# Performance work log

Hardware: AMD Instinct MI355X
Metric: run time of the kernel (lower is better)

The kernel has to match this reference:

```python
import jax, jax.numpy as jnp
import numpy as np

N = 262144
C = 4096  # number of clusters


def _segment_max(x, seg, num_segments):
    # global_max_pool: per-cluster max over points
    return jax.ops.segment_max(x, seg, num_segments=num_segments)


def setup_inputs() -> dict:
    key = jax.random.key(0)
    ks = jax.random.split(key, 16)

    def lin(k, fan_in, fan_out):
        bound = 1.0 / np.sqrt(fan_in)
        kw, kb = jax.random.split(k)
        W = jax.random.uniform(kw, (fan_in, fan_out), jnp.float32, -bound, bound)
        b = jax.random.uniform(kb, (fan_out,), jnp.float32, -bound, bound)
        return W, b

    relative_points = jax.random.normal(ks[0], (N, 3), jnp.float32)
    features = jax.random.normal(ks[1], (N, 64), jnp.float32)
    cluster = jax.random.randint(ks[2], (N,), 0, C, jnp.int64)

    enc_W1, enc_b1 = lin(ks[3], 3, 32)    # neighborhood encoder MLP
    enc_W2, enc_b2 = lin(ks[4], 32, 64)
    W1, b1 = lin(ks[5], 3 + 64 + 64, 128)  # fc_layers (input_size + enc_out + 3)
    W2, b2 = lin(ks[6], 128, 128)
    G1, gb1 = lin(ks[7], 128, 128)          # fc_layers_global
    G2, gb2 = lin(ks[8], 128, 256)

    return dict(relative_points=relative_points, features=features, cluster=cluster,
                enc_W1=enc_W1, enc_b1=enc_b1, enc_W2=enc_W2, enc_b2=enc_b2,
                W1=W1, b1=b1, W2=W2, b2=b2, G1=G1, gb1=gb1, G2=G2, gb2=gb2)


def reference(relative_points, features, cluster,
              enc_W1, enc_b1, enc_W2, enc_b2,
              W1, b1, W2, b2, G1, gb1, G2, gb2):
    # --- neighborhood encoder: per-point MLP then per-cluster max-pool ---
    h = jax.nn.relu(relative_points @ enc_W1 + enc_b1)          # [N, 32]
    h = jax.nn.relu(h @ enc_W2 + enc_b2)                        # [N, 64]
    neigh_enc = _segment_max(h, cluster, C)                     # [C, 64]

    # gather-by-index duplication + concat
    dup = neigh_enc[cluster]                                    # [N, 64]
    encoded = jnp.concatenate([relative_points, features, dup], axis=1)  # [N, 131]

    # local fc stack (relu, leaky=False)
    encoded = jax.nn.relu(encoded @ W1 + b1)                    # [N, 128]
    encoded = jax.nn.relu(encoded @ W2 + b2)                    # [N, 128]

    # global_max_pool (mean=False)
    encoded_global = _segment_max(encoded, cluster, C)          # [C, 128]

    # global fc stack
    encoded_global = jax.nn.relu(encoded_global @ G1 + gb1)     # [C, 128]
    encoded_global = jax.nn.relu(encoded_global @ G2 + gb2)     # [C, 256]
    return encoded_global
```

## Files before the change

### kernel.cpp

```cpp
#include <hip/hip_runtime.h>

#define NN 262144
#define CC 4096
#define NBLK 64
#define PPB (NN / NBLK)
#define NT (NN / 64)
#define SLOTS 3

typedef __attribute__((ext_vector_type(8))) short bf16x8;
typedef __attribute__((ext_vector_type(4))) float f32x4;

__device__ __forceinline__ unsigned short f_to_bf16u(float f) {
  union { float f; unsigned u; } v; v.f = f;
  unsigned u = v.u;
  u += 0x7fffu + ((u >> 16) & 1u);
  return (unsigned short)(u >> 16);
}
__device__ __forceinline__ unsigned pk2(float a, float b) {
  return (unsigned)f_to_bf16u(a) | ((unsigned)f_to_bf16u(b) << 16);
}

__global__ __launch_bounds__(256) void k_hist(
    const int* __restrict__ cluster, unsigned* __restrict__ hist2d)
{
  __shared__ unsigned h[CC];
  const int t = threadIdx.x, b = blockIdx.x;
  for (int q = t; q < CC; q += 256) h[q] = 0u;
  __syncthreads();
  const int base = b * PPB;
#pragma unroll 4
  for (int k = 0; k < PPB; k += 256) atomicAdd(&h[cluster[base + k + t]], 1u);
  __syncthreads();
  for (int q = t; q < CC; q += 256) hist2d[b * CC + q] = h[q];
}

__global__ __launch_bounds__(256) void k_scan_a(
    const unsigned* __restrict__ hist2d, unsigned* __restrict__ base2d,
    unsigned* __restrict__ totals)
{
  const int c = blockIdx.x * 256 + threadIdx.x;
  unsigned acc = 0;
#pragma unroll 4
  for (int b = 0; b < NBLK; ++b) {
    const unsigned v = hist2d[b * CC + c];
    base2d[b * CC + c] = acc;
    acc += v;
  }
  totals[c] = acc;
}

__global__ __launch_bounds__(256) void k_scan_b(
    const unsigned* __restrict__ totals, unsigned* __restrict__ cstart)
{
  __shared__ unsigned part[256];
  const int t = threadIdx.x;
  unsigned loc[16];
  unsigned s = 0;
#pragma unroll
  for (int q = 0; q < 16; ++q) { loc[q] = s; s += totals[t * 16 + q]; }
  part[t] = s;
  __syncthreads();
  for (int off = 1; off < 256; off <<= 1) {
    const unsigned v = (t >= off) ? part[t - off] : 0u;
    __syncthreads();
    part[t] += v;
    __syncthreads();
  }
  const unsigned baset = part[t] - s;
#pragma unroll
  for (int q = 0; q < 16; ++q) cstart[t * 16 + q] = baset + loc[q];
}

__global__ __launch_bounds__(256) void k_scatter(
    const int* __restrict__ cluster, const unsigned* __restrict__ base2d,
    const unsigned* __restrict__ cstart, unsigned* __restrict__ perm,
    unsigned* __restrict__ scid)
{
  __shared__ unsigned cur[CC];
  const int t = threadIdx.x, b = blockIdx.x;
  for (int q = t; q < CC; q += 256) cur[q] = base2d[b * CC + q] + cstart[q];
  __syncthreads();
  const int base = b * PPB;
#pragma unroll 4
  for (int k = 0; k < PPB; k += 256) {
    const int i = base + k + t;
    const int c = cluster[i];
    const unsigned pos = atomicAdd(&cur[c], 1u);
    perm[pos] = (unsigned)i;
    scid[pos] = (unsigned)c;
  }
}

__global__ __launch_bounds__(256) void k_pack(
    const float* __restrict__ eW2, const float* __restrict__ W1,
    const float* __restrict__ W2, unsigned* __restrict__ packE,
    unsigned* __restrict__ pack1, unsigned* __restrict__ pack2)
{
  const int id = blockIdx.x * 256 + threadIdx.x;
  if (id < 1024) {
    const int nt = id >> 8, l = (id >> 2) & 63, v = id & 3;
    const int k0 = (l >> 4) * 8 + 2 * v, col = nt * 16 + (l & 15);
    packE[id] = pk2(eW2[k0 * 64 + col], eW2[(k0 + 1) * 64 + col]);
  } else if (id < 1024 + 6144) {
    const int j = id - 1024;
    const int kk = j >> 11, nt = (j >> 8) & 7, l = (j >> 2) & 63, v = j & 3;
    const int col = nt * 16 + (l & 15);
    float vals[2];
#pragma unroll
    for (int h = 0; h < 2; ++h) {
      const int k = kk * 32 + (l >> 4) * 8 + 2 * v + h;
      vals[h] = (k < 64) ? W1[(3 + k) * 128 + col]
              : (k < 67) ? W1[(k - 64) * 128 + col] : 0.f;
    }
    pack1[j] = pk2(vals[0], vals[1]);
  } else if (id < 1024 + 6144 + 8192) {
    const int j = id - (1024 + 6144);
    const int kk = j >> 11, nt = (j >> 8) & 7, l = (j >> 2) & 63, v = j & 3;
    const int col = nt * 16 + (l & 15);
    const int k0 = kk * 32 + (l >> 4) * 4 + v;
    pack2[j] = pk2(W2[k0 * 128 + col], W2[(k0 + 16) * 128 + col]);
  }
}

__global__ __launch_bounds__(256) void k_enc_t(
    const float* __restrict__ pts, const unsigned* __restrict__ perm,
    const unsigned* __restrict__ scid, const unsigned* __restrict__ cstart,
    const float* __restrict__ eW1, const float* __restrict__ eb1,
    const float* __restrict__ eb2, const unsigned* __restrict__ packE,
    float* __restrict__ pse)
{
  __shared__ float P4[64 * 4];
  __shared__ unsigned h1s[64 * 20];
  __shared__ int seg_r0[65];
  __shared__ int seg_cid[64];
  __shared__ int seg_j[64];
  __shared__ int nseg_s;
  const int t = threadIdx.x;
  const int lane = t & 63, w = t >> 6;
  const int g = lane >> 4, ln15 = lane & 15;
  const int b = blockIdx.x;

  if (w == 0) {
    const int cid = (int)scid[b * 64 + t];
    const bool flag = (t == 0) || ((int)scid[b * 64 + t - 1] != cid);
    const unsigned long long mask = __ballot(flag);
    const int rank = (int)__popcll(mask & ((1ull << t) - 1ull));
    if (flag) {
      seg_r0[rank] = t;
      seg_cid[rank] = cid;
      seg_j[rank] = b - (int)(cstart[cid] >> 6);
    }
    if (t == 0) {
      const int ns = (int)__popcll(mask);
      nseg_s = ns;
      seg_r0[ns] = 64;
    }
    const int i = (int)perm[b * 64 + t];
    P4[t * 4 + 0] = pts[i * 3 + 0];
    P4[t * 4 + 1] = pts[i * 3 + 1];
    P4[t * 4 + 2] = pts[i * 3 + 2];
    P4[t * 4 + 3] = 0.f;
  }
  __syncthreads();
  {
    const int r = t >> 2, qq = t & 3;
    const float p0 = P4[r * 4], p1 = P4[r * 4 + 1], p2 = P4[r * 4 + 2];
    unsigned wv[4];
#pragma unroll
    for (int u = 0; u < 4; ++u) {
      float hv[2];
#pragma unroll
      for (int hh = 0; hh < 2; ++hh) {
        const int cc2 = qq * 8 + 2 * u + hh;
        hv[hh] = fmaxf(fmaf(p2, eW1[64 + cc2],
                       fmaf(p1, eW1[32 + cc2],
                       fmaf(p0, eW1[cc2], eb1[cc2]))), 0.f);
      }
      wv[u] = pk2(hv[0], hv[1]);
    }
    uint4 st; st.x = wv[0]; st.y = wv[1]; st.z = wv[2]; st.w = wv[3];
    *reinterpret_cast<uint4*>(&h1s[r * 20 + qq * 4]) = st;
  }
  __syncthreads();
  {
    const int col = w * 16 + ln15;
    const bf16x8 bfr = *reinterpret_cast<const bf16x8*>(&packE[(w * 64 + lane) * 4]);
    const float bias = eb2[col];
    f32x4 acc[4];
#pragma unroll
    for (int m = 0; m < 4; ++m) acc[m] = f32x4{bias, bias, bias, bias};
#pragma unroll
    for (int m = 0; m < 4; ++m) {
      const bf16x8 a = *reinterpret_cast<const bf16x8*>(&h1s[(16 * m + ln15) * 20 + g * 4]);
      acc[m] = __builtin_amdgcn_mfma_f32_16x16x32_bf16(a, bfr, acc[m], 0, 0, 0);
    }
    const int nseg = nseg_s;
    for (int s = 0; s < nseg; ++s) {
      const int r0 = seg_r0[s], r1 = seg_r0[s + 1];
      float v = 0.f;
#pragma unroll
      for (int m = 0; m < 4; ++m)
#pragma unroll
        for (int q = 0; q < 4; ++q) {
          const int row = 16 * m + 4 * g + q;
          const bool in = (row >= r0) & (row < r1);
          v = fmaxf(v, in ? fmaxf(acc[m][q], 0.f) : 0.f);
        }
      v = fmaxf(v, __shfl_xor(v, 16, 64));
      v = fmaxf(v, __shfl_xor(v, 32, 64));
      if (lane < 16) {
        const int c = seg_cid[s], j = seg_j[s];
        if (j < SLOTS - 1)
          pse[((size_t)c * SLOTS + j) * 64 + col] = v;
        else
          atomicMax((int*)&pse[((size_t)c * SLOTS + (SLOTS - 1)) * 64 + col],
                    __float_as_int(v));
      }
    }
  }
}

__global__ __launch_bounds__(256) void k_cproj2(
    const float* __restrict__ pse, const float* __restrict__ W1,
    const float* __restrict__ b1, float* __restrict__ cproj)
{
  __shared__ float nm2[2][64];
  const int t = threadIdx.x, b = blockIdx.x;
  if (t < 128) {
    const int rr = t >> 6, col = t & 63;
    const float* p = pse + ((size_t)(b * 2 + rr) * SLOTS) * 64 + col;
    nm2[rr][col] = fmaxf(fmaxf(p[0], p[64]), p[128]);
  }
  __syncthreads();
  const int rr = t >> 7, col = t & 127;
  const float* __restrict__ Wd = W1 + 67 * 128;
  float a = b1[col];
#pragma unroll 4
  for (int j = 0; j < 16; ++j) {
    const f32x4 nv = *reinterpret_cast<const f32x4*>(&nm2[rr][4 * j]);
    a = fmaf(nv[0], Wd[(4 * j + 0) * 128 + col], a);
    a = fmaf(nv[1], Wd[(4 * j + 1) * 128 + col], a);
    a = fmaf(nv[2], Wd[(4 * j + 2) * 128 + col], a);
    a = fmaf(nv[3], Wd[(4 * j + 3) * 128 + col], a);
  }
  cproj[(size_t)(b * 2 + rr) * 128 + col] = a;
}

__global__ __launch_bounds__(256) void k_fc_t(
    const float* __restrict__ pts, const float* __restrict__ feat,
    const unsigned* __restrict__ perm, const unsigned* __restrict__ scid,
    const unsigned* __restrict__ cstart, const float* __restrict__ b2,
    const float* __restrict__ cproj, const unsigned* __restrict__ pack1,
    const unsigned* __restrict__ pack2, float* __restrict__ psf)
{
  __shared__ unsigned buf[64 * 68];
  __shared__ float cpd[16][128];
  __shared__ int ridx_l[64];
  __shared__ int cid_l[64];
  __shared__ int seg_r0[65];
  __shared__ int seg_cid[64];
  __shared__ int seg_j[64];
  __shared__ int nseg_s;
  const int t = threadIdx.x;
  const int lane = t & 63, w = t >> 6;
  const int g = lane >> 4, ln15 = lane & 15;
  const int b = blockIdx.x;

  if (w == 0) {
    const int cid = (int)scid[b * 64 + t];
    cid_l[t] = cid;
    const bool flag = (t == 0) || ((int)scid[b * 64 + t - 1] != cid);
    const unsigned long long mask = __ballot(flag);
    const int rank = (int)__popcll(mask & ((1ull << t) - 1ull));
    ridx_l[t] = (int)__popcll(mask & ((2ull << t) - 1ull)) - 1;
    if (flag) {
      seg_r0[rank] = t;
      seg_cid[rank] = cid;
      seg_j[rank] = b - (int)(cstart[cid] >> 6);
    }
    if (t == 0) {
      const int ns = (int)__popcll(mask);
      nseg_s = ns;
      seg_r0[ns] = 64;
    }
  }
  {
    const int r = t >> 2, seg = t & 3;
    const int i = (int)perm[b * 64 + r];
    const float4* __restrict__ fp = reinterpret_cast<const float4*>(&feat[(size_t)i * 64 + seg * 16]);
    const float4 f0 = fp[0], f1 = fp[1], f2 = fp[2], f3 = fp[3];
    uint4 s0v, s1v;
    s0v.x = pk2(f0.x, f0.y); s0v.y = pk2(f0.z, f0.w);
    s0v.z = pk2(f1.x, f1.y); s0v.w = pk2(f1.z, f1.w);
    s1v.x = pk2(f2.x, f2.y); s1v.y = pk2(f2.z, f2.w);
    s1v.z = pk2(f3.x, f3.y); s1v.w = pk2(f3.z, f3.w);
    *reinterpret_cast<uint4*>(&buf[r * 52 + seg * 8 + 0]) = s0v;
    *reinterpret_cast<uint4*>(&buf[r * 52 + seg * 8 + 4]) = s1v;
  }
  if (t < 64) {
    const int i = (int)perm[b * 64 + t];
    uint4 pw;
    pw.x = pk2(pts[i * 3 + 0], pts[i * 3 + 1]);
    pw.y = pk2(pts[i * 3 + 2], 0.f);
    pw.z = 0u; pw.w = 0u;
    uint4 zz; zz.x = zz.y = zz.z = zz.w = 0u;
    *reinterpret_cast<uint4*>(&buf[t * 52 + 32]) = pw;
    *reinterpret_cast<uint4*>(&buf[t * 52 + 36]) = zz;
    *reinterpret_cast<uint4*>(&buf[t * 52 + 40]) = zz;
    *reinterpret_cast<uint4*>(&buf[t * 52 + 44]) = zz;
  }
  __syncthreads();
  {
    const int nseg = nseg_s;
    const int lim = (nseg < 16) ? nseg : 16;
    for (int s = t >> 7; s < lim; s += 2)
      cpd[s][t & 127] = cproj[(size_t)seg_cid[s] * 128 + (t & 127)];
  }
  __syncthreads();

  const int colA = w * 32 + ln15, colB = colA + 16;
  f32x4 acc0[4], acc1[4];
  {
    const int nseg = nseg_s;
    if (nseg <= 2) {
      const float cA0 = cpd[0][colA], cA1 = cpd[0][colB];
      const float cB0 = (nseg == 2) ? cpd[1][colA] : cA0;
      const float cB1 = (nseg == 2) ? cpd[1][colB] : cA1;
      const int rb = (nseg == 2) ? seg_r0[1] : 64;
#pragma unroll
      for (int m = 0; m < 4; ++m)
#pragma unroll
        for (int q = 0; q < 4; ++q) {
          const int row = 16 * m + 4 * g + q;
          acc0[m][q] = (row < rb) ? cA0 : cB0;
          acc1[m][q] = (row < rb) ? cA1 : cB1;
        }
    } else {
#pragma unroll
      for (int m = 0; m < 4; ++m)
#pragma unroll
        for (int q = 0; q < 4; ++q) {
          const int row = 16 * m + 4 * g + q;
          const int idx = ridx_l[row];
          if (idx < 16) {
            acc0[m][q] = cpd[idx][colA];
            acc1[m][q] = cpd[idx][colB];
          } else {
            const int cc = cid_l[row];
            acc0[m][q] = cproj[(size_t)cc * 128 + colA];
            acc1[m][q] = cproj[(size_t)cc * 128 + colB];
          }
        }
    }
  }
  {
#pragma unroll
    for (int kk = 0; kk < 3; ++kk) {
      const bf16x8 bf0 = *reinterpret_cast<const bf16x8*>(&pack1[((kk * 8 + 2 * w + 0) * 64 + lane) * 4]);
      const bf16x8 bf1 = *reinterpret_cast<const bf16x8*>(&pack1[((kk * 8 + 2 * w + 1) * 64 + lane) * 4]);
#pragma unroll
      for (int m = 0; m < 4; ++m) {
        const bf16x8 a = *reinterpret_cast<const bf16x8*>(&buf[(16 * m + ln15) * 52 + kk * 16 + g * 4]);
        acc0[m] = __builtin_amdgcn_mfma_f32_16x16x32_bf16(a, bf0, acc0[m], 0, 0, 0);
        acc1[m] = __builtin_amdgcn_mfma_f32_16x16x32_bf16(a, bf1, acc1[m], 0, 0, 0);
      }
    }
  }
  __syncthreads();
  {
#pragma unroll
    for (int m = 0; m < 4; ++m)
#pragma unroll
      for (int q = 0; q < 4; ++q) {
        const int row = 16 * m + 4 * g + q;
        buf[row * 68 + w * 16 + ln15] =
            pk2(fmaxf(acc0[m][q], 0.f), fmaxf(acc1[m][q], 0.f));
      }
  }
  __syncthreads();
  {
    const float bb0 = b2[colA], bb1 = b2[colB];
#pragma unroll
    for (int m = 0; m < 4; ++m) {
      acc0[m] = f32x4{bb0, bb0, bb0, bb0};
      acc1[m] = f32x4{bb1, bb1, bb1, bb1};
    }
#pragma unroll
    for (int kk = 0; kk < 4; ++kk) {
      const bf16x8 bf0 = *reinterpret_cast<const bf16x8*>(&pack2[((kk * 8 + 2 * w + 0) * 64 + lane) * 4]);
      const bf16x8 bf1 = *reinterpret_cast<const bf16x8*>(&pack2[((kk * 8 + 2 * w + 1) * 64 + lane) * 4]);
#pragma unroll
      for (int m = 0; m < 4; ++m) {
        const bf16x8 a = *reinterpret_cast<const bf16x8*>(&buf[(16 * m + ln15) * 68 + kk * 16 + g * 4]);
        acc0[m] = __builtin_amdgcn_mfma_f32_16x16x32_bf16(a, bf0, acc0[m], 0, 0, 0);
        acc1[m] = __builtin_amdgcn_mfma_f32_16x16x32_bf16(a, bf1, acc1[m], 0, 0, 0);
      }
    }
  }
  {
    const int nseg = nseg_s;
    for (int s = 0; s < nseg; ++s) {
      const int r0 = seg_r0[s], r1 = seg_r0[s + 1];
      float v0 = 0.f, v1 = 0.f;
#pragma unroll
      for (int m = 0; m < 4; ++m)
#pragma unroll
        for (int q = 0; q < 4; ++q) {
          const int row = 16 * m + 4 * g + q;
          const bool in = (row >= r0) & (row < r1);
          v0 = fmaxf(v0, in ? fmaxf(acc0[m][q], 0.f) : 0.f);
          v1 = fmaxf(v1, in ? fmaxf(acc1[m][q], 0.f) : 0.f);
        }
      v0 = fmaxf(v0, __shfl_xor(v0, 16, 64)); v0 = fmaxf(v0, __shfl_xor(v0, 32, 64));
      v1 = fmaxf(v1, __shfl_xor(v1, 16, 64)); v1 = fmaxf(v1, __shfl_xor(v1, 32, 64));
      if (lane < 16) {
        const int c = seg_cid[s], j = seg_j[s];
        if (j < SLOTS - 1) {
          psf[((size_t)c * SLOTS + j) * 128 + colA] = v0;
          psf[((size_t)c * SLOTS + j) * 128 + colB] = v1;
        } else {
          atomicMax((int*)&psf[((size_t)c * SLOTS + (SLOTS - 1)) * 128 + colA], __float_as_int(v0));
          atomicMax((int*)&psf[((size_t)c * SLOTS + (SLOTS - 1)) * 128 + colB], __float_as_int(v1));
        }
      }
    }
  }
}

__global__ __launch_bounds__(256) void k_glob(
    const float* __restrict__ psf, const float* __restrict__ G1,
    const float* __restrict__ gb1, const float* __restrict__ G2,
    const float* __restrict__ gb2, float* __restrict__ out)
{
  __shared__ float pooled[128];
  __shared__ float part[256];
  __shared__ float tg[128];
  const int t = threadIdx.x, c = blockIdx.x;
  if (t < 128) {
    const float* p = psf + (size_t)c * SLOTS * 128 + t;
    pooled[t] = fmaxf(fmaxf(p[0], p[128]), p[256]);
  }
  __syncthreads();
  {
    const int col = t & 127, half = t >> 7;
    float a = half ? 0.f : gb1[col];
#pragma unroll 2
    for (int j = 0; j < 16; ++j) {
      const f32x4 pv = *reinterpret_cast<const f32x4*>(&pooled[half * 64 + 4 * j]);
      a = fmaf(pv[0], G1[(half * 64 + 4 * j + 0) * 128 + col], a);
      a = fmaf(pv[1], G1[(half * 64 + 4 * j + 1) * 128 + col], a);
      a = fmaf(pv[2], G1[(half * 64 + 4 * j + 2) * 128 + col], a);
      a = fmaf(pv[3], G1[(half * 64 + 4 * j + 3) * 128 + col], a);
    }
    part[t] = a;
  }
  __syncthreads();
  if (t < 128) tg[t] = fmaxf(part[t] + part[t + 128], 0.f);
  __syncthreads();
  {
    float a = gb2[t];
#pragma unroll 2
    for (int j = 0; j < 32; ++j) {
      const f32x4 tv = *reinterpret_cast<const f32x4*>(&tg[4 * j]);
      a = fmaf(tv[0], G2[(4 * j + 0) * 256 + t], a);
      a = fmaf(tv[1], G2[(4 * j + 1) * 256 + t], a);
      a = fmaf(tv[2], G2[(4 * j + 2) * 256 + t], a);
      a = fmaf(tv[3], G2[(4 * j + 3) * 256 + t], a);
    }
    out[(size_t)c * 256 + t] = fmaxf(a, 0.f);
  }
}

extern "C" void kernel_launch(void* const* d_in, const int* in_sizes, int n_in,
                              void* d_out, int out_size, void* d_ws, size_t ws_size,
                              hipStream_t stream)
{
  (void)in_sizes; (void)n_in; (void)out_size; (void)ws_size;
  const float* pts  = (const float*)d_in[0];
  const float* feat = (const float*)d_in[1];
  const int*   clus = (const int*)  d_in[2];
  const float* eW1  = (const float*)d_in[3];
  const float* eb1  = (const float*)d_in[4];
  const float* eW2  = (const float*)d_in[5];
  const float* eb2  = (const float*)d_in[6];
  const float* W1   = (const float*)d_in[7];
  const float* b1   = (const float*)d_in[8];
  const float* W2   = (const float*)d_in[9];
  const float* b2   = (const float*)d_in[10];
  const float* G1   = (const float*)d_in[11];
  const float* gb1  = (const float*)d_in[12];
  const float* G2   = (const float*)d_in[13];
  const float* gb2  = (const float*)d_in[14];
  float* out = (float*)d_out;

  unsigned* ws      = (unsigned*)d_ws;
  unsigned* hist2d  = ws;
  unsigned* base2d  = ws + 262144;
  float*    pse     = (float*)ws;
  unsigned* totals  = ws + 786432;
  unsigned* cstart  = ws + 790528;
  unsigned* perm    = ws + 794624;
  unsigned* scid    = ws + 1056768;
  unsigned* packE   = ws + 1318912;
  unsigned* pack1   = ws + 1319936;
  unsigned* pack2   = ws + 1326080;
  float*    cproj   = (float*)(ws + 1334272);
  float*    psf     = (float*)(ws + 1858560);

  k_hist   <<<NBLK, 256, 0, stream>>>(clus, hist2d);
  k_scan_a <<<CC / 256, 256, 0, stream>>>(hist2d, base2d, totals);
  k_scan_b <<<1, 256, 0, stream>>>(totals, cstart);
  k_scatter<<<NBLK, 256, 0, stream>>>(clus, base2d, cstart, perm, scid);
  k_pack   <<<60, 256, 0, stream>>>(eW2, W1, W2, packE, pack1, pack2);
  hipMemsetAsync((void*)pse, 0, (size_t)786432 * 4, stream);
  hipMemsetAsync((void*)psf, 0, (size_t)1572864 * 4, stream);
  k_enc_t  <<<NT, 256, 0, stream>>>(pts, perm, scid, cstart, eW1, eb1, eb2, packE, pse);
  k_cproj2 <<<CC / 2, 256, 0, stream>>>(pse, W1, b1, cproj);
  k_fc_t   <<<NT, 256, 0, stream>>>(pts, feat, perm, scid, cstart, b2, cproj,
                                    pack1, pack2, psf);
  k_glob   <<<CC, 256, 0, stream>>>(psf, G1, gb1, G2, gb2, out);
}
```

Baseline: 125.3 us.

## Fuse preprocessing kernels to cut launches and fold psf memset into scan

```diff
diff --git a/kernel.cpp b/kernel.cpp
--- a/kernel.cpp
+++ b/kernel.cpp
@@ -1,4 +1,5 @@
 #include <hip/hip_runtime.h>
+#include <hip/hip_bf16.h>
 
 #define NN 262144
 #define CC 4096
@@ -10,93 +11,34 @@
 typedef __attribute__((ext_vector_type(8))) short bf16x8;
 typedef __attribute__((ext_vector_type(4))) float f32x4;
 
-__device__ __forceinline__ unsigned short f_to_bf16u(float f) {
-  union { float f; unsigned u; } v; v.f = f;
-  unsigned u = v.u;
-  u += 0x7fffu + ((u >> 16) & 1u);
-  return (unsigned short)(u >> 16);
-}
 __device__ __forceinline__ unsigned pk2(float a, float b) {
-  return (unsigned)f_to_bf16u(a) | ((unsigned)f_to_bf16u(b) << 16);
-}
-
-__global__ __launch_bounds__(256) void k_hist(
-    const int* __restrict__ cluster, unsigned* __restrict__ hist2d)
-{
-  __shared__ unsigned h[CC];
-  const int t = threadIdx.x, b = blockIdx.x;
-  for (int q = t; q < CC; q += 256) h[q] = 0u;
-  __syncthreads();
-  const int base = b * PPB;
-#pragma unroll 4
-  for (int k = 0; k < PPB; k += 256) atomicAdd(&h[cluster[base + k + t]], 1u);
-  __syncthreads();
-  for (int q = t; q < CC; q += 256) hist2d[b * CC + q] = h[q];
-}
-
-__global__ __launch_bounds__(256) void k_scan_a(
-    const unsigned* __restrict__ hist2d, unsigned* __restrict__ base2d,
-    unsigned* __restrict__ totals)
-{
-  const int c = blockIdx.x * 256 + threadIdx.x;
-  unsigned acc = 0;
-#pragma unroll 4
-  for (int b = 0; b < NBLK; ++b) {
-    const unsigned v = hist2d[b * CC + c];
-    base2d[b * CC + c] = acc;
-    acc += v;
-  }
-  totals[c] = acc;
-}
-
-__global__ __launch_bounds__(256) void k_scan_b(
-    const unsigned* __restrict__ totals, unsigned* __restrict__ cstart)
-{
-  __shared__ unsigned part[256];
-  const int t = threadIdx.x;
-  unsigned loc[16];
-  unsigned s = 0;
-#pragma unroll
-  for (int q = 0; q < 16; ++q) { loc[q] = s; s += totals[t * 16 + q]; }
-  part[t] = s;
-  __syncthreads();
-  for (int off = 1; off < 256; off <<= 1) {
-    const unsigned v = (t >= off) ? part[t - off] : 0u;
-    __syncthreads();
-    part[t] += v;
-    __syncthreads();
-  }
-  const unsigned baset = part[t] - s;
-#pragma unroll
-  for (int q = 0; q < 16; ++q) cstart[t * 16 + q] = baset + loc[q];
-}
-
-__global__ __launch_bounds__(256) void k_scatter(
-    const int* __restrict__ cluster, const unsigned* __restrict__ base2d,
-    const unsigned* __restrict__ cstart, unsigned* __restrict__ perm,
-    unsigned* __restrict__ scid)
-{
-  __shared__ unsigned cur[CC];
-  const int t = threadIdx.x, b = blockIdx.x;
-  for (int q = t; q < CC; q += 256) cur[q] = base2d[b * CC + q] + cstart[q];
-  __syncthreads();
-  const int base = b * PPB;
-#pragma unroll 4
-  for (int k = 0; k < PPB; k += 256) {
-    const int i = base + k + t;
-    const int c = cluster[i];
-    const unsigned pos = atomicAdd(&cur[c], 1u);
-    perm[pos] = (unsigned)i;
-    scid[pos] = (unsigned)c;
-  }
-}
-
-__global__ __launch_bounds__(256) void k_pack(
+  __hip_bfloat16 ha = __float2bfloat16(a);
+  __hip_bfloat16 hb = __float2bfloat16(b);
+  unsigned short ua, ub;
+  __builtin_memcpy(&ua, &ha, 2);
+  __builtin_memcpy(&ub, &hb, 2);
+  return (unsigned)ua | ((unsigned)ub << 16);
+}
+
+__global__ __launch_bounds__(256) void k_init(
+    const int* __restrict__ cluster, unsigned* __restrict__ hist2d,
     const float* __restrict__ eW2, const float* __restrict__ W1,
     const float* __restrict__ W2, unsigned* __restrict__ packE,
     unsigned* __restrict__ pack1, unsigned* __restrict__ pack2)
 {
-  const int id = blockIdx.x * 256 + threadIdx.x;
+  __shared__ unsigned h[CC];
+  const int t = threadIdx.x, b = blockIdx.x;
+  if (b < NBLK) {
+    for (int q = t; q < CC; q += 256) h[q] = 0u;
+    __syncthreads();
+    const int base = b * PPB;
+#pragma unroll 4
+    for (int k = 0; k < PPB; k += 256) atomicAdd(&h[cluster[base + k + t]], 1u);
+    __syncthreads();
+    for (int q = t; q < CC; q += 256) hist2d[b * CC + q] = h[q];
+    return;
+  }
+  const int id = (b - NBLK) * 256 + t;
   if (id < 1024) {
     const int nt = id >> 8, l = (id >> 2) & 63, v = id & 3;
     const int k0 = (l >> 4) * 8 + 2 * v, col = nt * 16 + (l & 15);
@@ -107,18 +49,81 @@
     const int col = nt * 16 + (l & 15);
     float vals[2];
 #pragma unroll
-    for (int h = 0; h < 2; ++h) {
-      const int k = kk * 32 + (l >> 4) * 8 + 2 * v + h;
-      vals[h] = (k < 64) ? W1[(3 + k) * 128 + col]
-              : (k < 67) ? W1[(k - 64) * 128 + col] : 0.f;
+    for (int hh = 0; hh < 2; ++hh) {
+      const int k = kk * 32 + (l >> 4) * 8 + 2 * v + hh;
+      vals[hh] = (k < 64) ? W1[(3 + k) * 128 + col]
+               : (k < 67) ? W1[(k - 64) * 128 + col] : 0.f;
     }
     pack1[j] = pk2(vals[0], vals[1]);
-  } else if (id < 1024 + 6144 + 8192) {
+  } else {
     const int j = id - (1024 + 6144);
     const int kk = j >> 11, nt = (j >> 8) & 7, l = (j >> 2) & 63, v = j & 3;
     const int col = nt * 16 + (l & 15);
     const int k0 = kk * 32 + (l >> 4) * 4 + v;
     pack2[j] = pk2(W2[k0 * 128 + col], W2[(k0 + 16) * 128 + col]);
+  }
+}
+
+__global__ __launch_bounds__(256) void k_scan_a(
+    const unsigned* __restrict__ hist2d, unsigned* __restrict__ base2d,
+    unsigned* __restrict__ totals, float4* __restrict__ psf4)
+{
+  const int t = threadIdx.x, b = blockIdx.x;
+  if (b < 16) {
+    const int c = b * 256 + t;
+    unsigned acc = 0;
+#pragma unroll 4
+    for (int bb = 0; bb < NBLK; ++bb) {
+      const unsigned v = hist2d[bb * CC + c];
+      base2d[bb * CC + c] = acc;
+      acc += v;
+    }
+    totals[c] = acc;
+  } else {
+    const int zb = b - 16;
+    const float4 z = {0.f, 0.f, 0.f, 0.f};
+    float4* __restrict__ p = psf4 + (size_t)zb * 8192 + t;
+#pragma unroll 8
+    for (int q = 0; q < 32; ++q) p[q * 256] = z;
+  }
+}
+
+__global__ __launch_bounds__(256) void k_scatter(
+    const int* __restrict__ cluster, const unsigned* __restrict__ base2d,
+    const unsigned* __restrict__ totals, unsigned* __restrict__ perm,
+    unsigned* __restrict__ scid, unsigned* __restrict__ cstart_g)
+{
+  __shared__ unsigned cur[CC];
+  __shared__ unsigned part[256];
+  const int t = threadIdx.x, b = blockIdx.x;
+  unsigned loc[16];
+  unsigned s = 0;
+#pragma unroll
+  for (int q = 0; q < 16; ++q) { loc[q] = s; s += totals[t * 16 + q]; }
+  part[t] = s;
+  __syncthreads();
+  for (int off = 1; off < 256; off <<= 1) {
+    const unsigned v = (t >= off) ? part[t - off] : 0u;
+    __syncthreads();
+    part[t] += v;
+    __syncthreads();
+  }
+  const unsigned baset = part[t] - s;
+#pragma unroll
+  for (int q = 0; q < 16; ++q) {
+    const unsigned cs = baset + loc[q];
+    cur[t * 16 + q] = base2d[b * CC + t * 16 + q] + cs;
+    if (b == 0) cstart_g[t * 16 + q] = cs;
+  }
+  __syncthreads();
+  const int base = b * PPB;
+#pragma unroll 4
+  for (int k = 0; k < PPB; k += 256) {
+    const int i = base + k + t;
+    const int c = cluster[i];
+    const unsigned pos = atomicAdd(&cur[c], 1u);
+    perm[pos] = (unsigned)i;
+    scid[pos] = (unsigned)c;
   }
 }
 
@@ -254,7 +259,7 @@
     const unsigned* __restrict__ pack2, float* __restrict__ psf)
 {
   __shared__ unsigned buf[64 * 68];
-  __shared__ float cpd[16][128];
+  __shared__ float cpd[8][128];
   __shared__ int ridx_l[64];
   __shared__ int cid_l[64];
   __shared__ int seg_r0[65];
@@ -312,7 +317,7 @@
   __syncthreads();
   {
     const int nseg = nseg_s;
-    const int lim = (nseg < 16) ? nseg : 16;
+    const int lim = (nseg < 8) ? nseg : 8;
     for (int s = t >> 7; s < lim; s += 2)
       cpd[s][t & 127] = cproj[(size_t)seg_cid[s] * 128 + (t & 127)];
   }
@@ -342,7 +347,7 @@
         for (int q = 0; q < 4; ++q) {
           const int row = 16 * m + 4 * g + q;
           const int idx = ridx_l[row];
-          if (idx < 16) {
+          if (idx < 8) {
             acc0[m][q] = cpd[idx][colA];
             acc1[m][q] = cpd[idx][colB];
           } else {
@@ -507,13 +512,11 @@
   float*    cproj   = (float*)(ws + 1334272);
   float*    psf     = (float*)(ws + 1858560);
 
-  k_hist   <<<NBLK, 256, 0, stream>>>(clus, hist2d);
-  k_scan_a <<<CC / 256, 256, 0, stream>>>(hist2d, base2d, totals);
-  k_scan_b <<<1, 256, 0, stream>>>(totals, cstart);
-  k_scatter<<<NBLK, 256, 0, stream>>>(clus, base2d, cstart, perm, scid);
-  k_pack   <<<60, 256, 0, stream>>>(eW2, W1, W2, packE, pack1, pack2);
+  k_init   <<<NBLK + 60, 256, 0, stream>>>(clus, hist2d, eW2, W1, W2,
+                                           packE, pack1, pack2);
+  k_scan_a <<<64, 256, 0, stream>>>(hist2d, base2d, totals, (float4*)psf);
+  k_scatter<<<NBLK, 256, 0, stream>>>(clus, base2d, totals, perm, scid, cstart);
   hipMemsetAsync((void*)pse, 0, (size_t)786432 * 4, stream);
-  hipMemsetAsync((void*)psf, 0, (size_t)1572864 * 4, stream);
   k_enc_t  <<<NT, 256, 0, stream>>>(pts, perm, scid, cstart, eW1, eb1, eb2, packE, pse);
   k_cproj2 <<<CC / 2, 256, 0, stream>>>(pse, W1, b1, cproj);
   k_fc_t   <<<NT, 256, 0, stream>>>(pts, feat, perm, scid, cstart, b2, cproj,
```

New measurement: 119.0 us. 1.05x faster.
